# Kernel tuning notes

Measured on AMD Instinct MI355X. Metric: run time of the kernel, lower is better.

Reference implementation:

```python
import jax, jax.numpy as jnp
import numpy as np

B, S, D, H = 4, 2048, 1024, 16
DK = D // H


def setup_inputs() -> dict:
    key = jax.random.key(0)
    ks = jax.random.split(key, 9)
    x = jax.random.normal(ks[0], (B, S, D), dtype=jnp.float32)
    scale = 1.0 / np.sqrt(D)
    wq = jax.random.normal(ks[1], (D, D), dtype=jnp.float32) * scale
    wk = jax.random.normal(ks[2], (D, D), dtype=jnp.float32) * scale
    wv = jax.random.normal(ks[3], (D, D), dtype=jnp.float32) * scale
    wo = jax.random.normal(ks[4], (D, D), dtype=jnp.float32) * scale
    bq = jax.random.normal(ks[5], (D,), dtype=jnp.float32) * 0.01
    bk = jax.random.normal(ks[6], (D,), dtype=jnp.float32) * 0.01
    bv = jax.random.normal(ks[7], (D,), dtype=jnp.float32) * 0.01
    bo = jax.random.normal(ks[8], (D,), dtype=jnp.float32) * 0.01
    # causal mask: True where scores should be masked to -inf (j > i)
    mask = jnp.triu(jnp.ones((S, S), dtype=bool), k=1)[None, None, :, :]
    return {"x": x, "wq": wq, "bq": bq, "wk": wk, "bk": bk,
            "wv": wv, "bv": bv, "wo": wo, "bo": bo, "mask": mask}


def reference(x, wq, bq, wk, bk, wv, bv, wo, bo, mask):
    b, s, _ = x.shape
    # projections
    q = (x @ wq + bq).reshape(b, s, H, DK).transpose(0, 2, 1, 3)  # [B,H,S,DK]
    k = (x @ wk + bk).reshape(b, s, H, DK).transpose(0, 2, 1, 3)
    v = (x @ wv + bv).reshape(b, s, H, DK).transpose(0, 2, 1, 3)
    scores = jnp.einsum("bhqd,bhkd->bhqk", q, k) / np.sqrt(DK)
    scores = jnp.where(mask, -jnp.inf, scores)
    attn = jax.nn.softmax(scores, axis=-1)  # dropout p=0.0 -> identity
    out = jnp.einsum("bhqk,bhkd->bhqd", attn, v)
    out = out.transpose(0, 2, 1, 3).reshape(b, s, D)
    return out @ wo + bo
```

## Files before the change

kernel.cpp:

```cpp
#include <hip/hip_runtime.h>


typedef __attribute__((ext_vector_type(8))) short short8;
typedef __attribute__((ext_vector_type(4))) float floatx4;
typedef __attribute__((ext_vector_type(4))) unsigned short ushort4v;

#define SCLF (0.125f * 1.44269504f)

__device__ __forceinline__ unsigned short f2bf(float f) {
    unsigned int u = __float_as_uint(f);
    unsigned int r = (u + 0x7fffu + ((u >> 16) & 1u)) >> 16;
    return (unsigned short)r;
}

__device__ __forceinline__ unsigned int pk2bf(float lo, float hi) {
    return __builtin_amdgcn_perm(__float_as_uint(hi), __float_as_uint(lo), 0x07060302u);
}

__device__ __forceinline__ void gll16(const unsigned short* g, unsigned short* l) {
    __builtin_amdgcn_global_load_lds(
        (const __attribute__((address_space(1))) unsigned int*)g,
        (__attribute__((address_space(3))) unsigned int*)l, 16, 0, 0);
}

__device__ __forceinline__ void xcd_tile(int nx, int& m0, int& n0) {
    int lid = blockIdx.y * nx + blockIdx.x;
    int grp = lid & 7;
    int inner = lid >> 3;
    int m_per = (gridDim.y + 7) >> 3;
    int my = grp * m_per + inner / nx;
    int mx = inner % nx;
    m0 = my * 128; n0 = mx * 128;
}

__global__ void cvtx_kernel(const float* __restrict__ x, unsigned short* __restrict__ xb) {
    int i = (blockIdx.x * 256 + threadIdx.x) * 4;
    float4 v = *(const float4*)&x[i];
    ushort4v o;
    o.x = f2bf(v.x); o.y = f2bf(v.y); o.z = f2bf(v.z); o.w = f2bf(v.w);
    *(ushort4v*)&xb[i] = o;
}

__global__ void wtrans_kernel(const float* __restrict__ wq, const float* __restrict__ wk,
                              const float* __restrict__ wv, const float* __restrict__ wo,
                              unsigned short* __restrict__ wtbase) {
    __shared__ float t[32][33];
    int z = blockIdx.z;
    const float* w = (z == 0) ? wq : (z == 1) ? wk : (z == 2) ? wv : wo;
    unsigned short* wt = wtbase + ((long)z << 20);
    int kb = blockIdx.y * 32, nb = blockIdx.x * 32;
    int col = threadIdx.x & 31, rw = threadIdx.x >> 5;
#pragma unroll
    for (int i = 0; i < 4; i++) {
        int row = rw + i * 8;
        t[row][col] = w[(kb + row) * 1024 + nb + col];
    }
    __syncthreads();
#pragma unroll
    for (int i = 0; i < 4; i++) {
        int row = rw + i * 8;
        wt[(nb + row) * 1024 + kb + col] = f2bf(t[col][row]);
    }
}

__device__ __forceinline__ short8 ldsr(const unsigned short* p) { return *(const short8*)p; }

template <bool SW>
__device__ __forceinline__ void gemm_core(const unsigned short* __restrict__ A,
                                          const unsigned short* __restrict__ Bt,
                                          unsigned short* As, unsigned short* Bs,
                                          int m0, int n0, int K, floatx4 (&acc)[4][4]) {
    int tid = threadIdx.x;
    int lane = tid & 63, wave = tid >> 6;
    int wr = wave >> 1, wc = wave & 1;
    int quad = lane >> 4, l15 = lane & 15, l7 = l15 & 7;
    int rsub = lane >> 3;
    int gl = (lane & 7) ^ rsub;
    floatx4 zero4 = {0.f, 0.f, 0.f, 0.f};
#pragma unroll
    for (int i = 0; i < 4; i++)
#pragma unroll
        for (int j = 0; j < 4; j++) acc[i][j] = zero4;

    for (int k0 = 0; k0 < K; k0 += 64) {
#pragma unroll
        for (int p = 0; p < 4; p++) {
            int idx = (wave * 4 + p) * 64 + lane;
            int row = (wave * 4 + p) * 8 + rsub;
            gll16(&A[(m0 + row) * K + k0 + gl * 8], &As[idx * 8]);
            gll16(&Bt[(n0 + row) * K + k0 + gl * 8], &Bs[idx * 8]);
        }
        __syncthreads();
#pragma unroll
        for (int kk = 0; kk < 2; kk++) {
            short8 af[4], bf[4];
#pragma unroll
            for (int mt = 0; mt < 4; mt++) {
                int r = wr * 64 + mt * 16 + l15;
                af[mt] = ldsr(&As[r * 64 + (((kk * 4 + quad) ^ l7) * 8)]);
            }
#pragma unroll
            for (int nt = 0; nt < 4; nt++) {
                int r = wc * 64 + nt * 16 + l15;
                bf[nt] = ldsr(&Bs[r * 64 + (((kk * 4 + quad) ^ l7) * 8)]);
            }
#pragma unroll
            for (int mt = 0; mt < 4; mt++)
#pragma unroll
                for (int nt = 0; nt < 4; nt++) {
                    if (SW)
                        acc[mt][nt] = __builtin_amdgcn_mfma_f32_16x16x32_bf16(bf[nt], af[mt], acc[mt][nt], 0, 0, 0);
                    else
                        acc[mt][nt] = __builtin_amdgcn_mfma_f32_16x16x32_bf16(af[mt], bf[nt], acc[mt][nt], 0, 0, 0);
                }
        }
        __syncthreads();
    }
}

__global__ __launch_bounds__(256) void proj_kernel(
    const unsigned short* __restrict__ xb, const unsigned short* __restrict__ wt,
    const float* __restrict__ bq, const float* __restrict__ bk, const float* __restrict__ bv,
    unsigned short* __restrict__ qo, unsigned short* __restrict__ ko,
    unsigned short* __restrict__ vo) {
    __shared__ __align__(16) unsigned short As[128 * 64];
    __shared__ __align__(16) unsigned short Bs[128 * 64];
    int m0, n0;
    xcd_tile(24, m0, n0);
    floatx4 acc[4][4];
    int tid = threadIdx.x, lane = tid & 63, wave = tid >> 6;
    int wr = wave >> 1, wc = wave & 1, quad = lane >> 4, l15 = lane & 15;

    if (n0 < 2048) {
        gemm_core<true>(xb, wt, As, Bs, m0, n0, 1024, acc);
        int which = n0 >> 10;
        const float* bias = which ? bk : bq;
        unsigned short* dst = which ? ko : qo;
        float sc = which ? 1.0f : SCLF;
#pragma unroll
        for (int mt = 0; mt < 4; mt++)
#pragma unroll
            for (int nt = 0; nt < 4; nt++) {
                int tok = m0 + wr * 64 + mt * 16 + l15;
                int b = tok >> 11, s = tok & 2047;
                int colf = (n0 + wc * 64 + nt * 16 + quad * 4) & 1023;
                float4 bb = *(const float4*)&bias[colf];
                int h = colf >> 6, dk = colf & 63;
                ushort4v o;
                o.x = f2bf((acc[mt][nt][0] + bb.x) * sc);
                o.y = f2bf((acc[mt][nt][1] + bb.y) * sc);
                o.z = f2bf((acc[mt][nt][2] + bb.z) * sc);
                o.w = f2bf((acc[mt][nt][3] + bb.w) * sc);
                *(ushort4v*)&dst[((long)((b * 16 + h) * 2048 + s)) * 64 + dk] = o;
            }
    } else {
        gemm_core<false>(xb, wt, As, Bs, m0, n0, 1024, acc);
#pragma unroll
        for (int mt = 0; mt < 4; mt++)
#pragma unroll
            for (int nt = 0; nt < 4; nt++) {
                int tok0 = m0 + wr * 64 + mt * 16 + quad * 4;
                int b = tok0 >> 11, s = tok0 & 2047;
                int colf = (n0 & 1023) + wc * 64 + nt * 16 + l15;
                int h = colf >> 6, dk = colf & 63;
                float bb = bv[colf];
                ushort4v o;
                o.x = f2bf(acc[mt][nt][0] + bb);
                o.y = f2bf(acc[mt][nt][1] + bb);
                o.z = f2bf(acc[mt][nt][2] + bb);
                o.w = f2bf(acc[mt][nt][3] + bb);
                *(ushort4v*)&vo[((long)((b * 16 + h) * 64 + dk)) * 2048 + s] = o;
            }
    }
}

__global__ __launch_bounds__(256) void gemm_out_kernel(
    const unsigned short* __restrict__ ob, const unsigned short* __restrict__ wto,
    const float* __restrict__ bo, float* __restrict__ out) {
    __shared__ __align__(16) unsigned short As[128 * 64];
    __shared__ __align__(16) unsigned short Bs[128 * 64];
    int m0, n0;
    xcd_tile(8, m0, n0);
    floatx4 acc[4][4];
    gemm_core<true>(ob, wto, As, Bs, m0, n0, 1024, acc);

    int tid = threadIdx.x, lane = tid & 63, wave = tid >> 6;
    int wr = wave >> 1, wc = wave & 1, quad = lane >> 4, l15 = lane & 15;
#pragma unroll
    for (int mt = 0; mt < 4; mt++)
#pragma unroll
        for (int nt = 0; nt < 4; nt++) {
            int tok = m0 + wr * 64 + mt * 16 + l15;
            int cg = n0 + wc * 64 + nt * 16 + quad * 4;
            float4 bb = *(const float4*)&bo[cg];
            float4 o;
            o.x = acc[mt][nt][0] + bb.x;
            o.y = acc[mt][nt][1] + bb.y;
            o.z = acc[mt][nt][2] + bb.z;
            o.w = acc[mt][nt][3] + bb.w;
            *(float4*)&out[(long)tok * 1024 + cg] = o;
        }
}

__device__ __forceinline__ void stage_kv(const unsigned short* __restrict__ Kg,
                                         const unsigned short* __restrict__ Vg,
                                         unsigned short* Ks, unsigned short* Vs,
                                         int lane, int wave) {
    int rsub = lane >> 3;
    int g = (lane & 7) ^ rsub;
#pragma unroll
    for (int p = 0; p < 2; p++) {
        int chunk = wave * 2 + p;
        int r = chunk * 8 + rsub;
        gll16(&Kg[r * 64 + g * 8], &Ks[chunk * 512]);
        gll16(&Vg[r * 2048 + g * 8], &Vs[chunk * 512]);
    }
}

__global__ __launch_bounds__(256, 4) void attn_kernel(
    const unsigned short* __restrict__ Q, const unsigned short* __restrict__ Kk,
    const unsigned short* __restrict__ Vt, unsigned short* __restrict__ O) {
    __shared__ __align__(16) unsigned short Ks[2][8 * 512];
    __shared__ __align__(16) unsigned short Vs[2][8 * 512];
    __shared__ __align__(16) unsigned short Ps[4 * 16 * 64];

    int bid = blockIdx.x;
    int qt = 15 - (bid >> 6);
    int bh = bid & 63;
    int q0 = qt * 128;
    long base = (long)bh * 2048 * 64;
    long vbase = (long)bh * 64 * 2048;
    int tid = threadIdx.x, lane = tid & 63, wave = tid >> 6;
    int quad = lane >> 4, l15 = lane & 15, l7 = l15 & 7;

    short8 qfA[2], qfB[2];
    int qrA = q0 + wave * 16 + l15;
    int qrB = qrA + 64;
    qfA[0] = *(const short8*)&Q[base + qrA * 64 + quad * 8];
    qfA[1] = *(const short8*)&Q[base + qrA * 64 + 32 + quad * 8];
    qfB[0] = *(const short8*)&Q[base + qrB * 64 + quad * 8];
    qfB[1] = *(const short8*)&Q[base + qrB * 64 + 32 + quad * 8];

    float lA = 0.f, lB = 0.f;
    floatx4 oA[4], oB[4];
    floatx4 zero4 = {0.f, 0.f, 0.f, 0.f};
#pragma unroll
    for (int st = 0; st < 4; st++) { oA[st] = zero4; oB[st] = zero4; }

    unsigned short* myP = &Ps[(wave * 16) * 64];
    int pw_off = l15 * 64 + (quad & 1) * 4;
    int pr0 = l15 * 64 + ((quad ^ l7) * 8);
    int pr1 = l15 * 64 + (((4 + quad) ^ l7) * 8);

    int ktmax = 2 * qt + 1;
    stage_kv(&Kk[base], &Vt[vbase], Ks[0], Vs[0], lane, wave);
    __syncthreads();

    for (int kt = 0; kt <= ktmax; kt++) {
        int cur = kt & 1;
        if (kt < ktmax)
            stage_kv(&Kk[base + (long)(kt + 1) * 64 * 64], &Vt[vbase + (kt + 1) * 64],
                     Ks[cur ^ 1], Vs[cur ^ 1], lane, wave);
        bool doA = (kt < ktmax);
        bool maskA = (kt == ktmax - 1);
        bool maskB = (kt == ktmax);

        floatx4 saA[4], saB[4];
#pragma unroll
        for (int st = 0; st < 4; st++) {
            int row = st * 16 + l15;
            short8 kf0 = ldsr(&Ks[cur][row * 64 + ((quad ^ l7) * 8)]);
            short8 kf1 = ldsr(&Ks[cur][row * 64 + (((4 + quad) ^ l7) * 8)]);
            saB[st] = __builtin_amdgcn_mfma_f32_16x16x32_bf16(kf0, qfB[0], zero4, 0, 0, 0);
            saB[st] = __builtin_amdgcn_mfma_f32_16x16x32_bf16(kf1, qfB[1], saB[st], 0, 0, 0);
            if (doA) {
                saA[st] = __builtin_amdgcn_mfma_f32_16x16x32_bf16(kf0, qfA[0], zero4, 0, 0, 0);
                saA[st] = __builtin_amdgcn_mfma_f32_16x16x32_bf16(kf1, qfA[1], saA[st], 0, 0, 0);
            }
        }

        int kg0 = kt * 64 + quad * 4;
        short8 pfB0, pfB1, pfA0, pfA1;
        {
            float p[4][4];
#pragma unroll
            for (int st = 0; st < 4; st++)
#pragma unroll
                for (int r = 0; r < 4; r++)
                    p[st][r] = __builtin_amdgcn_exp2f(saB[st][r]);
            if (maskB) {
#pragma unroll
                for (int st = 0; st < 4; st++)
#pragma unroll
                    for (int r = 0; r < 4; r++)
                        if (kg0 + st * 16 + r > qrB) p[st][r] = 0.f;
            }
            float rs = 0.f;
#pragma unroll
            for (int st = 0; st < 4; st++) {
                rs += p[st][0] + p[st][1] + p[st][2] + p[st][3];
                uint2 pw;
                pw.x = pk2bf(p[st][0], p[st][1]);
                pw.y = pk2bf(p[st][2], p[st][3]);
                *(uint2*)&myP[pw_off + (((st * 2 + (quad >> 1)) ^ l7) * 8)] = pw;
            }
            rs += __shfl_xor(rs, 16, 64);
            rs += __shfl_xor(rs, 32, 64);
            lB += rs;
            pfB0 = ldsr(&myP[pr0]);
            pfB1 = ldsr(&myP[pr1]);
        }
        if (doA) {
            float p[4][4];
#pragma unroll
            for (int st = 0; st < 4; st++)
#pragma unroll
                for (int r = 0; r < 4; r++)
                    p[st][r] = __builtin_amdgcn_exp2f(saA[st][r]);
            if (maskA) {
#pragma unroll
                for (int st = 0; st < 4; st++)
#pragma unroll
                    for (int r = 0; r < 4; r++)
                        if (kg0 + st * 16 + r > qrA) p[st][r] = 0.f;
            }
            float rs = 0.f;
#pragma unroll
            for (int st = 0; st < 4; st++) {
                rs += p[st][0] + p[st][1] + p[st][2] + p[st][3];
                uint2 pw;
                pw.x = pk2bf(p[st][0], p[st][1]);
                pw.y = pk2bf(p[st][2], p[st][3]);
                *(uint2*)&myP[pw_off + (((st * 2 + (quad >> 1)) ^ l7) * 8)] = pw;
            }
            rs += __shfl_xor(rs, 16, 64);
            rs += __shfl_xor(rs, 32, 64);
            lA += rs;
            pfA0 = ldsr(&myP[pr0]);
            pfA1 = ldsr(&myP[pr1]);
        }

#pragma unroll
        for (int st = 0; st < 4; st++) {
            int row = st * 16 + l15;
            short8 vf0 = ldsr(&Vs[cur][row * 64 + ((quad ^ l7) * 8)]);
            short8 vf1 = ldsr(&Vs[cur][row * 64 + (((4 + quad) ^ l7) * 8)]);
            oB[st] = __builtin_amdgcn_mfma_f32_16x16x32_bf16(vf0, pfB0, oB[st], 0, 0, 0);
            oB[st] = __builtin_amdgcn_mfma_f32_16x16x32_bf16(vf1, pfB1, oB[st], 0, 0, 0);
            if (doA) {
                oA[st] = __builtin_amdgcn_mfma_f32_16x16x32_bf16(vf0, pfA0, oA[st], 0, 0, 0);
                oA[st] = __builtin_amdgcn_mfma_f32_16x16x32_bf16(vf1, pfA1, oA[st], 0, 0, 0);
            }
        }
        __syncthreads();
    }

    int b = bh >> 4, h = bh & 15;
    float invA = 1.f / lA, invB = 1.f / lB;
#pragma unroll
    for (int st = 0; st < 4; st++) {
        uint2 ov;
        ov.x = pk2bf(oA[st][0] * invA, oA[st][1] * invA);
        ov.y = pk2bf(oA[st][2] * invA, oA[st][3] * invA);
        *(uint2*)&O[((long)(b * 2048 + qrA)) * 1024 + h * 64 + st * 16 + quad * 4] = ov;
        uint2 ow;
        ow.x = pk2bf(oB[st][0] * invB, oB[st][1] * invB);
        ow.y = pk2bf(oB[st][2] * invB, oB[st][3] * invB);
        *(uint2*)&O[((long)(b * 2048 + qrB)) * 1024 + h * 64 + st * 16 + quad * 4] = ow;
    }
}

extern "C" void kernel_launch(void* const* d_in, const int* in_sizes, int n_in,
                              void* d_out, int out_size, void* d_ws, size_t ws_size,
                              hipStream_t stream) {
    const float* x  = (const float*)d_in[0];
    const float* wq = (const float*)d_in[1];
    const float* bq = (const float*)d_in[2];
    const float* wk = (const float*)d_in[3];
    const float* bk = (const float*)d_in[4];
    const float* wv = (const float*)d_in[5];
    const float* bv = (const float*)d_in[6];
    const float* wo = (const float*)d_in[7];
    const float* bo = (const float*)d_in[8];

    char* w = (char*)d_ws;
    unsigned short* xb  = (unsigned short*)w;
    unsigned short* wtq = (unsigned short*)(w + (16u << 20));
    unsigned short* wto = wtq + (3u << 20);
    unsigned short* qb  = wto + (1u << 20);
    unsigned short* kb  = qb + (8u << 20);
    unsigned short* vb  = kb + (8u << 20);
    unsigned short* ob  = vb + (8u << 20);

    cvtx_kernel<<<8192, 256, 0, stream>>>(x, xb);
    wtrans_kernel<<<dim3(32, 32, 4), 256, 0, stream>>>(wq, wk, wv, wo, wtq);
    proj_kernel<<<dim3(24, 64), 256, 0, stream>>>(xb, wtq, bq, bk, bv, qb, kb, vb);
    attn_kernel<<<1024, 256, 0, stream>>>(qb, kb, vb, ob);
    gemm_out_kernel<<<dim3(8, 64), 256, 0, stream>>>(ob, wto, bo, (float*)d_out);
}
```

Measured before the change: 268.6 us.

## Use 256x128 double-buffered GEMM tiles with 8 waves for projections

Replaces the 128x128 single-buffered GEMM core used by the QKV projection and output projection with a 256x128 tile handled by 512 threads. The next two K-tiles are prefetched into double-buffered LDS through global_load_lds, with explicit vmcnt waits and s_setprio around the MFMA bursts. The aim is to hide global-load latency behind compute and to reuse each B tile across more rows. In exchange it needs 96KB of dynamic LDS per block, halves the grid size, and depends on hand-placed barriers and waitcnt being correct.

```diff
diff --git a/kernel.cpp b/kernel.cpp
--- a/kernel.cpp
+++ b/kernel.cpp
@@ -23,14 +23,13 @@
         (__attribute__((address_space(3))) unsigned int*)l, 16, 0, 0);
 }
 
-__device__ __forceinline__ void xcd_tile(int nx, int& m0, int& n0) {
+__device__ __forceinline__ void xcd_tile2(int nx, int& my, int& mx) {
     int lid = blockIdx.y * nx + blockIdx.x;
     int grp = lid & 7;
     int inner = lid >> 3;
     int m_per = (gridDim.y + 7) >> 3;
-    int my = grp * m_per + inner / nx;
-    int mx = inner % nx;
-    m0 = my * 128; n0 = mx * 128;
+    my = grp * m_per + inner / nx;
+    mx = inner % nx;
 }
 
 __global__ void cvtx_kernel(const float* __restrict__ x, unsigned short* __restrict__ xb) {
@@ -63,87 +62,143 @@
     }
 }
 
+#define ASZ (256 * 64)
+#define BSZ (128 * 64)
+
 __device__ __forceinline__ short8 ldsr(const unsigned short* p) { return *(const short8*)p; }
 
 template <bool SW>
-__device__ __forceinline__ void gemm_core(const unsigned short* __restrict__ A,
-                                          const unsigned short* __restrict__ Bt,
-                                          unsigned short* As, unsigned short* Bs,
-                                          int m0, int n0, int K, floatx4 (&acc)[4][4]) {
+__device__ __forceinline__ void gemm_core256(const unsigned short* __restrict__ A,
+                                             const unsigned short* __restrict__ Bt,
+                                             unsigned short* As, unsigned short* Bs,
+                                             int m0, int n0, floatx4 (&acc)[8][2]) {
+    const int K = 1024, NT = 16;
     int tid = threadIdx.x;
     int lane = tid & 63, wave = tid >> 6;
-    int wr = wave >> 1, wc = wave & 1;
+    int wm = wave >> 2, wn = wave & 3;
     int quad = lane >> 4, l15 = lane & 15, l7 = l15 & 7;
     int rsub = lane >> 3;
     int gl = (lane & 7) ^ rsub;
+
     floatx4 zero4 = {0.f, 0.f, 0.f, 0.f};
 #pragma unroll
-    for (int i = 0; i < 4; i++)
-#pragma unroll
-        for (int j = 0; j < 4; j++) acc[i][j] = zero4;
-
-    for (int k0 = 0; k0 < K; k0 += 64) {
+    for (int i = 0; i < 8; i++)
+#pragma unroll
+        for (int j = 0; j < 2; j++) acc[i][j] = zero4;
+
+    auto stage = [&](int kt, int buf) {
+        const unsigned short* Ag = A + (long)m0 * K + kt * 64;
+        const unsigned short* Bg = Bt + (long)n0 * K + kt * 64;
+        unsigned short* as = As + buf * ASZ;
+        unsigned short* bs = Bs + buf * BSZ;
 #pragma unroll
         for (int p = 0; p < 4; p++) {
-            int idx = (wave * 4 + p) * 64 + lane;
-            int row = (wave * 4 + p) * 8 + rsub;
-            gll16(&A[(m0 + row) * K + k0 + gl * 8], &As[idx * 8]);
-            gll16(&Bt[(n0 + row) * K + k0 + gl * 8], &Bs[idx * 8]);
-        }
-        __syncthreads();
-#pragma unroll
-        for (int kk = 0; kk < 2; kk++) {
-            short8 af[4], bf[4];
-#pragma unroll
-            for (int mt = 0; mt < 4; mt++) {
-                int r = wr * 64 + mt * 16 + l15;
-                af[mt] = ldsr(&As[r * 64 + (((kk * 4 + quad) ^ l7) * 8)]);
-            }
-#pragma unroll
-            for (int nt = 0; nt < 4; nt++) {
-                int r = wc * 64 + nt * 16 + l15;
-                bf[nt] = ldsr(&Bs[r * 64 + (((kk * 4 + quad) ^ l7) * 8)]);
-            }
-#pragma unroll
-            for (int mt = 0; mt < 4; mt++)
-#pragma unroll
-                for (int nt = 0; nt < 4; nt++) {
-                    if (SW)
-                        acc[mt][nt] = __builtin_amdgcn_mfma_f32_16x16x32_bf16(bf[nt], af[mt], acc[mt][nt], 0, 0, 0);
-                    else
-                        acc[mt][nt] = __builtin_amdgcn_mfma_f32_16x16x32_bf16(af[mt], bf[nt], acc[mt][nt], 0, 0, 0);
-                }
-        }
-        __syncthreads();
-    }
-}
-
-__global__ __launch_bounds__(256) void proj_kernel(
+            int chunk = wave * 4 + p;
+            gll16(&Ag[(chunk * 8 + rsub) * K + gl * 8], &as[chunk * 512 + lane * 8]);
+        }
+#pragma unroll
+        for (int p = 0; p < 2; p++) {
+            int chunk = wave * 2 + p;
+            gll16(&Bg[(chunk * 8 + rsub) * K + gl * 8], &bs[chunk * 512 + lane * 8]);
+        }
+    };
+
+    stage(0, 0);
+    stage(1, 1);
+    asm volatile("s_waitcnt vmcnt(6)" ::: "memory");
+    __builtin_amdgcn_s_barrier();
+    asm volatile("" ::: "memory");
+
+    for (int kt = 0; kt < NT; kt++) {
+        int buf = kt & 1;
+        const unsigned short* as = As + buf * ASZ;
+        const unsigned short* bs = Bs + buf * BSZ;
+        short8 bf[2][2], af[4][2], ag[4][2];
+#pragma unroll
+        for (int j = 0; j < 2; j++) {
+            int rb = wn * 32 + j * 16 + l15;
+#pragma unroll
+            for (int kk = 0; kk < 2; kk++)
+                bf[j][kk] = ldsr(&bs[rb * 64 + (((kk * 4 + quad) ^ l7) * 8)]);
+        }
+#pragma unroll
+        for (int i = 0; i < 4; i++) {
+            int r = wm * 128 + i * 16 + l15;
+#pragma unroll
+            for (int kk = 0; kk < 2; kk++)
+                af[i][kk] = ldsr(&as[r * 64 + (((kk * 4 + quad) ^ l7) * 8)]);
+        }
+        __builtin_amdgcn_s_setprio(1);
+#pragma unroll
+        for (int i = 0; i < 4; i++)
+#pragma unroll
+            for (int j = 0; j < 2; j++)
+#pragma unroll
+                for (int kk = 0; kk < 2; kk++)
+                    acc[i][j] = SW
+                        ? __builtin_amdgcn_mfma_f32_16x16x32_bf16(bf[j][kk], af[i][kk], acc[i][j], 0, 0, 0)
+                        : __builtin_amdgcn_mfma_f32_16x16x32_bf16(af[i][kk], bf[j][kk], acc[i][j], 0, 0, 0);
+        __builtin_amdgcn_s_setprio(0);
+#pragma unroll
+        for (int i = 0; i < 4; i++) {
+            int r = wm * 128 + 64 + i * 16 + l15;
+#pragma unroll
+            for (int kk = 0; kk < 2; kk++)
+                ag[i][kk] = ldsr(&as[r * 64 + (((kk * 4 + quad) ^ l7) * 8)]);
+        }
+        __builtin_amdgcn_s_setprio(1);
+#pragma unroll
+        for (int i = 0; i < 4; i++)
+#pragma unroll
+            for (int j = 0; j < 2; j++)
+#pragma unroll
+                for (int kk = 0; kk < 2; kk++)
+                    acc[4 + i][j] = SW
+                        ? __builtin_amdgcn_mfma_f32_16x16x32_bf16(bf[j][kk], ag[i][kk], acc[4 + i][j], 0, 0, 0)
+                        : __builtin_amdgcn_mfma_f32_16x16x32_bf16(ag[i][kk], bf[j][kk], acc[4 + i][j], 0, 0, 0);
+        __builtin_amdgcn_s_setprio(0);
+        asm volatile("" ::: "memory");
+        __builtin_amdgcn_s_barrier();
+        asm volatile("" ::: "memory");
+        if (kt + 2 < NT) {
+            stage(kt + 2, buf);
+            asm volatile("s_waitcnt vmcnt(6)" ::: "memory");
+        } else {
+            asm volatile("s_waitcnt vmcnt(0)" ::: "memory");
+        }
+        __builtin_amdgcn_s_barrier();
+        asm volatile("" ::: "memory");
+    }
+}
+
+__global__ __launch_bounds__(512, 2) void proj_kernel(
     const unsigned short* __restrict__ xb, const unsigned short* __restrict__ wt,
     const float* __restrict__ bq, const float* __restrict__ bk, const float* __restrict__ bv,
     unsigned short* __restrict__ qo, unsigned short* __restrict__ ko,
     unsigned short* __restrict__ vo) {
-    __shared__ __align__(16) unsigned short As[128 * 64];
-    __shared__ __align__(16) unsigned short Bs[128 * 64];
-    int m0, n0;
-    xcd_tile(24, m0, n0);
-    floatx4 acc[4][4];
+    extern __shared__ __align__(16) unsigned short smem[];
+    unsigned short* As = smem;
+    unsigned short* Bs = smem + 2 * ASZ;
+    int my, mx;
+    xcd_tile2(24, my, mx);
+    int m0 = my * 256, n0 = mx * 128;
     int tid = threadIdx.x, lane = tid & 63, wave = tid >> 6;
-    int wr = wave >> 1, wc = wave & 1, quad = lane >> 4, l15 = lane & 15;
+    int wm = wave >> 2, wn = wave & 3, quad = lane >> 4, l15 = lane & 15;
+    floatx4 acc[8][2];
 
     if (n0 < 2048) {
-        gemm_core<true>(xb, wt, As, Bs, m0, n0, 1024, acc);
+        gemm_core256<true>(xb, wt, As, Bs, m0, n0, acc);
         int which = n0 >> 10;
         const float* bias = which ? bk : bq;
         unsigned short* dst = which ? ko : qo;
         float sc = which ? 1.0f : SCLF;
 #pragma unroll
-        for (int mt = 0; mt < 4; mt++)
-#pragma unroll
-            for (int nt = 0; nt < 4; nt++) {
-                int tok = m0 + wr * 64 + mt * 16 + l15;
+        for (int mt = 0; mt < 8; mt++)
+#pragma unroll
+            for (int nt = 0; nt < 2; nt++) {
+                int tok = m0 + wm * 128 + mt * 16 + l15;
                 int b = tok >> 11, s = tok & 2047;
-                int colf = (n0 + wc * 64 + nt * 16 + quad * 4) & 1023;
+                int colf = (n0 + wn * 32 + nt * 16 + quad * 4) & 1023;
                 float4 bb = *(const float4*)&bias[colf];
                 int h = colf >> 6, dk = colf & 63;
                 ushort4v o;
@@ -154,14 +209,14 @@
                 *(ushort4v*)&dst[((long)((b * 16 + h) * 2048 + s)) * 64 + dk] = o;
             }
     } else {
-        gemm_core<false>(xb, wt, As, Bs, m0, n0, 1024, acc);
-#pragma unroll
-        for (int mt = 0; mt < 4; mt++)
-#pragma unroll
-            for (int nt = 0; nt < 4; nt++) {
-                int tok0 = m0 + wr * 64 + mt * 16 + quad * 4;
+        gemm_core256<false>(xb, wt, As, Bs, m0, n0, acc);
+#pragma unroll
+        for (int mt = 0; mt < 8; mt++)
+#pragma unroll
+            for (int nt = 0; nt < 2; nt++) {
+                int tok0 = m0 + wm * 128 + mt * 16 + quad * 4;
                 int b = tok0 >> 11, s = tok0 & 2047;
-                int colf = (n0 & 1023) + wc * 64 + nt * 16 + l15;
+                int colf = (n0 & 1023) + wn * 32 + nt * 16 + l15;
                 int h = colf >> 6, dk = colf & 63;
                 float bb = bv[colf];
                 ushort4v o;
@@ -174,24 +229,26 @@
     }
 }
 
-__global__ __launch_bounds__(256) void gemm_out_kernel(
+__global__ __launch_bounds__(512, 2) void gemm_out_kernel(
     const unsigned short* __restrict__ ob, const unsigned short* __restrict__ wto,
     const float* __restrict__ bo, float* __restrict__ out) {
-    __shared__ __align__(16) unsigned short As[128 * 64];
-    __shared__ __align__(16) unsigned short Bs[128 * 64];
-    int m0, n0;
-    xcd_tile(8, m0, n0);
-    floatx4 acc[4][4];
-    gemm_core<true>(ob, wto, As, Bs, m0, n0, 1024, acc);
-
+    extern __shared__ __align__(16) unsigned short smem[];
+    unsigned short* As = smem;
+    unsigned short* Bs = smem + 2 * ASZ;
+    int my, mx;
+    xcd_tile2(8, my, mx);
+    int m0 = my * 256, n0 = mx * 128;
     int tid = threadIdx.x, lane = tid & 63, wave = tid >> 6;
-    int wr = wave >> 1, wc = wave & 1, quad = lane >> 4, l15 = lane & 15;
-#pragma unroll
-    for (int mt = 0; mt < 4; mt++)
-#pragma unroll
-        for (int nt = 0; nt < 4; nt++) {
-            int tok = m0 + wr * 64 + mt * 16 + l15;
-            int cg = n0 + wc * 64 + nt * 16 + quad * 4;
+    int wm = wave >> 2, wn = wave & 3, quad = lane >> 4, l15 = lane & 15;
+    floatx4 acc[8][2];
+    gemm_core256<true>(ob, wto, As, Bs, m0, n0, acc);
+
+#pragma unroll
+    for (int mt = 0; mt < 8; mt++)
+#pragma unroll
+        for (int nt = 0; nt < 2; nt++) {
+            int tok = m0 + wm * 128 + mt * 16 + l15;
+            int cg = n0 + wn * 32 + nt * 16 + quad * 4;
             float4 bb = *(const float4*)&bo[cg];
             float4 o;
             o.x = acc[mt][nt][0] + bb.x;
@@ -394,7 +451,7 @@
 
     cvtx_kernel<<<8192, 256, 0, stream>>>(x, xb);
     wtrans_kernel<<<dim3(32, 32, 4), 256, 0, stream>>>(wq, wk, wv, wo, wtq);
-    proj_kernel<<<dim3(24, 64), 256, 0, stream>>>(xb, wtq, bq, bk, bv, qb, kb, vb);
+    proj_kernel<<<dim3(24, 32), 512, 96 * 1024, stream>>>(xb, wtq, bq, bk, bv, qb, kb, vb);
     attn_kernel<<<1024, 256, 0, stream>>>(qb, kb, vb, ob);
-    gemm_out_kernel<<<dim3(8, 64), 256, 0, stream>>>(ob, wto, bo, (float*)d_out);
-}
+    gemm_out_kernel<<<dim3(8, 32), 512, 96 * 1024, stream>>>(ob, wto, bo, (float*)d_out);
+}
```

Result: no change. 264.3 us (-1.6%).
